# Performance work log

Measured on AMD Instinct MI355X. Metric: run time of the kernel, lower is better.

The kernel has to match this reference:

```python
import jax, jax.numpy as jnp
import numpy as np

FL = 9       # filterlen
STRIDE = 1
B, CIN, COUT, T = 2, 16, 16, 2048


def hmul(p, q):
    """Hamilton product of quaternions stored in the last axis (..., 4).
    Equivalent to q2m(p, Qmt).matmul(q) in the torch code."""
    pw, px, py, pz = p[..., 0], p[..., 1], p[..., 2], p[..., 3]
    qw, qx, qy, qz = q[..., 0], q[..., 1], q[..., 2], q[..., 3]
    return jnp.stack([
        pw * qw - px * qx - py * qy - pz * qz,
        pw * qx + px * qw + py * qz - pz * qy,
        pw * qy - px * qz + py * qw + pz * qx,
        pw * qz + px * qy - py * qx + pz * qw,
    ], axis=-1)


def setup_inputs() -> dict:
    key = jax.random.key(0)
    k1, k2, k3, k4 = jax.random.split(key, 4)
    he = np.float32(np.sqrt(2.0 / FL / CIN))
    pdims = (1, COUT, CIN, 1, FL, 1)  # broadcast over quaternion axis
    x = jax.random.normal(k1, (B, CIN, T, 4, 1), dtype=jnp.float32)
    a = jax.random.normal(k2, pdims, dtype=jnp.float32) * he
    b = jax.random.normal(k3, pdims, dtype=jnp.float32) * np.float32(0.5)
    c = jax.random.normal(k4, pdims, dtype=jnp.float32) * np.float32(np.sqrt(1.378 ** 2 - 0.25))
    return {"x": x, "a": a, "b": b, "c": c}


def reference(x, a, b, c):
    # x: (B, Cin, T, 4, 1) -> drop trailing singleton, quaternion on last axis
    xq = x[..., 0]  # (B, Cin, T, 4)
    fl, s = FL, STRIDE
    T_in = xq.shape[2]
    T_out = (T_in - fl) // s + 1

    # unfold: sliding windows of length fl along time -> (B, Cin, T_out, fl, 4)
    idx = jnp.arange(T_out)[:, None] * s + jnp.arange(fl)[None, :]
    q = xq[:, :, idx]                      # (B, Cin, T_out, fl, 4)
    q = q[:, None]                         # (B, 1, Cin, T_out, fl, 4)

    # center element of each window -> (B, 1, Cin, T_out, 1, 4)
    qp = xq[:, :, fl // 2: fl // 2 + (T_out - 1) * s + 1: s]
    qp = qp[:, None, :, :, None, :]

    eye = jnp.array([1.0, 0.0, 0.0, 0.0], dtype=x.dtype)
    conj_sign = jnp.array([1.0, -1.0, -1.0, -1.0], dtype=x.dtype)

    # qpc: (B, Cout, Cin, T_out, fl, 4) -- c adds to the real part only
    qpc = qp + c * eye

    # res = qpc * (q * conj(qpc)) / |qpc|^2   (quaternion conjugation/rotation)
    inner = hmul(q, qpc * conj_sign)
    nsq = jnp.sum(qpc * qpc, axis=-1, keepdims=True)
    res = hmul(qpc, inner) / nsq

    # res = q * res + b * res ; scale by a
    res = hmul(q, res) + b * res
    res = res * a

    # sum over filterlen (axis 4) and in-channels (axis 2)
    out = res.sum(axis=(2, 4))             # (B, Cout, T_out, 4)
    return out[..., None]                  # (B, Cout, T_out, 4, 1)
```

## Files before the change

kernel.cpp:

```cpp
#include <hip/hip_runtime.h>

#define FL 9
#define CIN 16
#define COUT 16
#define T_IN 2048
#define T_OUT 2040
#define TTILE 64
#define XW (TTILE + FL - 1)

__global__ __launch_bounds__(256) void qconv_main(
    const float* __restrict__ x, const float* __restrict__ pa,
    const float* __restrict__ pb, const float* __restrict__ pc,
    float4* __restrict__ part)
{
    __shared__ float4 xs[4][XW];
    __shared__ float4 red[3][8][TTILE];

    const int bid    = blockIdx.x;
    const int cohalf = bid & 1;
    const int cinq   = (bid >> 1) & 3;
    const int tile   = (bid >> 3) & 31;
    const int b      = bid >> 8;
    const int t0     = tile * TTILE;

    const int tid = threadIdx.x;
    const int tl  = tid & 63;
    const int cl  = tid >> 6;
    const int cin = cinq * 4 + cl;

    {
        const float4* xg = (const float4*)x + (b * CIN + cin) * T_IN;
        for (int i = tl; i < XW; i += 64) {
            int t = t0 + i;
            if (t > T_IN - 1) t = T_IN - 1;
            xs[cl][i] = xg[t];
        }
    }
    __syncthreads();

    const float4 qp  = xs[cl][tl + 4];
    const float  qpw = qp.x;
    const float  vx = qp.y, vy = qp.z, vz = qp.w;
    const float  h  = vx * vx + vy * vy + vz * vz;

    const int cin_s = __builtin_amdgcn_readfirstlane(cin);
    const int cob   = cohalf * 8;

    float4 acc[8];
    #pragma unroll
    for (int co = 0; co < 8; ++co) acc[co] = make_float4(0.f, 0.f, 0.f, 0.f);

    #pragma unroll
    for (int j = 0; j < FL; ++j) {
        const float4 Q = xs[cl][tl + j];
        const float qw = Q.x, ux = Q.y, uy = Q.z, uz = Q.w;

        const float cx = vy * uz - vz * uy;
        const float cy = vz * ux - vx * uz;
        const float cz = vx * uy - vy * ux;
        const float d  = vx * ux + vy * uy + vz * uz;
        const float uu = ux * ux + uy * uy + uz * uz;

        const float a1x = cx + cx, a1y = cy + cy, a1z = cz + cz;
        const float d2  = d + d;
        const float a0w = qw * h;
        const float a0x = d2 * vx - h * ux;
        const float a0y = d2 * vy - h * uy;
        const float a0z = d2 * vz - h * uz;

        const float b2w = qw * qw - uu;
        const float q2  = qw + qw;
        const float b2x = q2 * ux, b2y = q2 * uy, b2z = q2 * uz;

        const float b1w = -(ux * a1x + uy * a1y + uz * a1z);
        const float e1x = uy * a1z - uz * a1y;
        const float e1y = uz * a1x - ux * a1z;
        const float e1z = ux * a1y - uy * a1x;
        const float b1x = qw * a1x + e1x;
        const float b1y = qw * a1y + e1y;
        const float b1z = qw * a1z + e1z;

        const float b0w = qw * a0w - (ux * a0x + uy * a0y + uz * a0z);
        const float e0x = uy * a0z - uz * a0y;
        const float e0y = uz * a0x - ux * a0z;
        const float e0z = ux * a0y - uy * a0x;
        const float b0x = qw * a0x + a0w * ux + e0x;
        const float b0y = qw * a0y + a0w * uy + e0y;
        const float b0z = qw * a0z + a0w * uz + e0z;

        #pragma unroll
        for (int co = 0; co < 8; ++co) {
            const int pidx = ((cob + co) * CIN + cin_s) * FL + j;
            const float av = pa[pidx], bv = pb[pidx], cv = pc[pidx];

            const float pw  = qpw + cv;
            const float p2  = pw * pw;
            const float nsq = p2 + h;
            float rn = __builtin_amdgcn_rcpf(nsq);
            rn = rn * (2.0f - nsq * rn);
            const float s = av * rn;

            const float f2w = __builtin_fmaf(bv, qw, b2w);
            const float f2x = __builtin_fmaf(bv, ux, b2x);
            const float f2y = __builtin_fmaf(bv, uy, b2y);
            const float f2z = __builtin_fmaf(bv, uz, b2z);
            const float f1x = __builtin_fmaf(bv, a1x, b1x);
            const float f1y = __builtin_fmaf(bv, a1y, b1y);
            const float f1z = __builtin_fmaf(bv, a1z, b1z);
            const float f0w = __builtin_fmaf(bv, a0w, b0w);
            const float f0x = __builtin_fmaf(bv, a0x, b0x);
            const float f0y = __builtin_fmaf(bv, a0y, b0y);
            const float f0z = __builtin_fmaf(bv, a0z, b0z);

            const float rw = __builtin_fmaf(f2w, p2, __builtin_fmaf(b1w, pw, f0w));
            const float rx = __builtin_fmaf(f2x, p2, __builtin_fmaf(f1x, pw, f0x));
            const float ry = __builtin_fmaf(f2y, p2, __builtin_fmaf(f1y, pw, f0y));
            const float rz = __builtin_fmaf(f2z, p2, __builtin_fmaf(f1z, pw, f0z));

            acc[co].x = __builtin_fmaf(rw, s, acc[co].x);
            acc[co].y = __builtin_fmaf(rx, s, acc[co].y);
            acc[co].z = __builtin_fmaf(ry, s, acc[co].z);
            acc[co].w = __builtin_fmaf(rz, s, acc[co].w);
        }
    }

    if (cl != 0) {
        #pragma unroll
        for (int co = 0; co < 8; ++co) red[cl - 1][co][tl] = acc[co];
    }
    __syncthreads();
    if (cl == 0) {
        const int t = t0 + tl;
        if (t < T_OUT) {
            #pragma unroll
            for (int co = 0; co < 8; ++co) {
                const float4 r0 = red[0][co][tl];
                const float4 r1 = red[1][co][tl];
                const float4 r2 = red[2][co][tl];
                float4 o;
                o.x = acc[co].x + r0.x + r1.x + r2.x;
                o.y = acc[co].y + r0.y + r1.y + r2.y;
                o.z = acc[co].z + r0.z + r1.z + r2.z;
                o.w = acc[co].w + r0.w + r1.w + r2.w;
                part[(cinq * 32 + b * 16 + cob + co) * 2048 + t] = o;
            }
        }
    }
}

__global__ __launch_bounds__(256) void qconv_reduce(
    const float4* __restrict__ part, float4* __restrict__ out)
{
    const int N = 2 * COUT * T_OUT;
    for (int i = blockIdx.x * 256 + threadIdx.x; i < N; i += gridDim.x * 256) {
        const int t  = i % T_OUT;
        const int bc = i / T_OUT;
        const float4 p0 = part[(0 * 32 + bc) * 2048 + t];
        const float4 p1 = part[(1 * 32 + bc) * 2048 + t];
        const float4 p2 = part[(2 * 32 + bc) * 2048 + t];
        const float4 p3 = part[(3 * 32 + bc) * 2048 + t];
        float4 o;
        o.x = (p0.x + p1.x) + (p2.x + p3.x);
        o.y = (p0.y + p1.y) + (p2.y + p3.y);
        o.z = (p0.z + p1.z) + (p2.z + p3.z);
        o.w = (p0.w + p1.w) + (p2.w + p3.w);
        out[i] = o;
    }
}

extern "C" void kernel_launch(void* const* d_in, const int* in_sizes, int n_in,
                              void* d_out, int out_size, void* d_ws, size_t ws_size,
                              hipStream_t stream) {
    const float* x  = (const float*)d_in[0];
    const float* pa = (const float*)d_in[1];
    const float* pb = (const float*)d_in[2];
    const float* pc = (const float*)d_in[3];
    float4* part = (float4*)d_ws;
    float4* out  = (float4*)d_out;

    qconv_main<<<dim3(512), dim3(256), 0, stream>>>(x, pa, pb, pc, part);
    qconv_reduce<<<dim3(256), dim3(256), 0, stream>>>(part, out);
}
```

Baseline: 76.05 us.

## Split output channels into quarters and stage filter params in shared memory

Each block now handles four output channels instead of eight, doubling the grid to 1024 blocks, and launch bounds request higher occupancy. Filter parameters a, b, c are packed into a shared float4 table instead of three scalar global loads per output channel and tap. The nine input window quaternions are also preloaded into registers. The aim is more parallelism across the 256 CUs and less global/scalar load traffic in the inner loop. The cost is that the per-tap quaternion prework is recomputed twice as often across blocks, and the shared reads of parameters are per-lane loads rather than scalar loads.

```diff
diff --git a/kernel.cpp b/kernel.cpp
--- a/kernel.cpp
+++ b/kernel.cpp
@@ -8,25 +8,27 @@
 #define TTILE 64
 #define XW (TTILE + FL - 1)
 
-__global__ __launch_bounds__(256) void qconv_main(
+__global__ __launch_bounds__(256, 4) void qconv_main(
     const float* __restrict__ x, const float* __restrict__ pa,
     const float* __restrict__ pb, const float* __restrict__ pc,
     float4* __restrict__ part)
 {
     __shared__ float4 xs[4][XW];
-    __shared__ float4 red[3][8][TTILE];
+    __shared__ float4 pp[4][4][FL];
+    __shared__ float4 red[3][4][TTILE];
 
     const int bid    = blockIdx.x;
-    const int cohalf = bid & 1;
-    const int cinq   = (bid >> 1) & 3;
-    const int tile   = (bid >> 3) & 31;
-    const int b      = bid >> 8;
+    const int coquad = bid & 3;
+    const int cinq   = (bid >> 2) & 3;
+    const int tile   = (bid >> 4) & 31;
+    const int b      = bid >> 9;
     const int t0     = tile * TTILE;
 
     const int tid = threadIdx.x;
     const int tl  = tid & 63;
     const int cl  = tid >> 6;
     const int cin = cinq * 4 + cl;
+    const int cob = coquad * 4;
 
     {
         const float4* xg = (const float4*)x + (b * CIN + cin) * T_IN;
@@ -36,24 +38,32 @@
             xs[cl][i] = xg[t];
         }
     }
+    if (tid < 4 * 4 * FL) {
+        const int co_l = tid / (4 * FL);
+        const int r    = tid - co_l * (4 * FL);
+        const int ci_l = r / FL;
+        const int j    = r - ci_l * FL;
+        const int pidx = ((cob + co_l) * CIN + (cinq * 4 + ci_l)) * FL + j;
+        pp[co_l][ci_l][j] = make_float4(pa[pidx], pb[pidx], pc[pidx], 0.0f);
+    }
     __syncthreads();
 
-    const float4 qp  = xs[cl][tl + 4];
+    float4 q[FL];
+    #pragma unroll
+    for (int j = 0; j < FL; ++j) q[j] = xs[cl][tl + j];
+
+    const float4 qp  = q[4];
     const float  qpw = qp.x;
     const float  vx = qp.y, vy = qp.z, vz = qp.w;
     const float  h  = vx * vx + vy * vy + vz * vz;
 
-    const int cin_s = __builtin_amdgcn_readfirstlane(cin);
-    const int cob   = cohalf * 8;
-
-    float4 acc[8];
+    float4 acc[4];
     #pragma unroll
-    for (int co = 0; co < 8; ++co) acc[co] = make_float4(0.f, 0.f, 0.f, 0.f);
+    for (int co = 0; co < 4; ++co) acc[co] = make_float4(0.f, 0.f, 0.f, 0.f);
 
     #pragma unroll
     for (int j = 0; j < FL; ++j) {
-        const float4 Q = xs[cl][tl + j];
-        const float qw = Q.x, ux = Q.y, uy = Q.z, uz = Q.w;
+        const float qw = q[j].x, ux = q[j].y, uy = q[j].z, uz = q[j].w;
 
         const float cx = vy * uz - vz * uy;
         const float cy = vz * ux - vx * uz;
@@ -73,25 +83,19 @@
         const float b2x = q2 * ux, b2y = q2 * uy, b2z = q2 * uz;
 
         const float b1w = -(ux * a1x + uy * a1y + uz * a1z);
-        const float e1x = uy * a1z - uz * a1y;
-        const float e1y = uz * a1x - ux * a1z;
-        const float e1z = ux * a1y - uy * a1x;
-        const float b1x = qw * a1x + e1x;
-        const float b1y = qw * a1y + e1y;
-        const float b1z = qw * a1z + e1z;
+        const float b1x = qw * a1x + (uy * a1z - uz * a1y);
+        const float b1y = qw * a1y + (uz * a1x - ux * a1z);
+        const float b1z = qw * a1z + (ux * a1y - uy * a1x);
 
         const float b0w = qw * a0w - (ux * a0x + uy * a0y + uz * a0z);
-        const float e0x = uy * a0z - uz * a0y;
-        const float e0y = uz * a0x - ux * a0z;
-        const float e0z = ux * a0y - uy * a0x;
-        const float b0x = qw * a0x + a0w * ux + e0x;
-        const float b0y = qw * a0y + a0w * uy + e0y;
-        const float b0z = qw * a0z + a0w * uz + e0z;
+        const float b0x = qw * a0x + a0w * ux + (uy * a0z - uz * a0y);
+        const float b0y = qw * a0y + a0w * uy + (uz * a0x - ux * a0z);
+        const float b0z = qw * a0z + a0w * uz + (ux * a0y - uy * a0x);
 
         #pragma unroll
-        for (int co = 0; co < 8; ++co) {
-            const int pidx = ((cob + co) * CIN + cin_s) * FL + j;
-            const float av = pa[pidx], bv = pb[pidx], cv = pc[pidx];
+        for (int co = 0; co < 4; ++co) {
+            const float4 p = pp[co][cl][j];
+            const float av = p.x, bv = p.y, cv = p.z;
 
             const float pw  = qpw + cv;
             const float p2  = pw * pw;
@@ -126,14 +130,14 @@
 
     if (cl != 0) {
         #pragma unroll
-        for (int co = 0; co < 8; ++co) red[cl - 1][co][tl] = acc[co];
+        for (int co = 0; co < 4; ++co) red[cl - 1][co][tl] = acc[co];
     }
     __syncthreads();
     if (cl == 0) {
         const int t = t0 + tl;
         if (t < T_OUT) {
             #pragma unroll
-            for (int co = 0; co < 8; ++co) {
+            for (int co = 0; co < 4; ++co) {
                 const float4 r0 = red[0][co][tl];
                 const float4 r1 = red[1][co][tl];
                 const float4 r2 = red[2][co][tl];
@@ -178,6 +182,6 @@
     float4* part = (float4*)d_ws;
     float4* out  = (float4*)d_out;
 
-    qconv_main<<<dim3(512), dim3(256), 0, stream>>>(x, pa, pb, pc, part);
+    qconv_main<<<dim3(1024), dim3(256), 0, stream>>>(x, pa, pb, pc, part);
     qconv_reduce<<<dim3(256), dim3(256), 0, stream>>>(part, out);
 }
```

Measured after the change: 199.9 us. 163% more time.
